# Optimization experiments

Hardware: AMD Instinct MI355X
Metric: run time of the kernel (lower is better)

Reference implementation:

```python
import jax, jax.numpy as jnp
import numpy as np

B, GX, GY = 4, 480, 360
C_IN, C_OUT = 64, 32
N = 480000

def setup_inputs() -> dict:
    key = jax.random.key(0)
    k1, k2, k3, k4, k5 = jax.random.split(key, 5)
    pt_fea = jax.random.normal(k1, (N, C_IN), dtype=jnp.float32)
    pt_ind = jax.random.randint(k2, (N, 2), 0, 360, dtype=jnp.int32)
    batch_idx = jax.random.randint(k3, (N,), 0, B, dtype=jnp.int32)
    W_comp = jax.random.normal(k4, (C_IN, C_OUT), dtype=jnp.float32) * 0.1
    b_comp = jax.random.normal(k5, (C_OUT,), dtype=jnp.float32) * 0.1
    return {"pt_fea": pt_fea, "pt_ind": pt_ind, "batch_idx": batch_idx,
            "W_comp": W_comp, "b_comp": b_comp}

def reference(pt_fea, pt_ind, batch_idx, W_comp, b_comp):
    # Linearized voxel key: (batch, x, y) -> flat segment id.
    # torch.unique + scatter_max over unique voxels followed by fancy-index
    # scatter into a zero grid is equivalent to a dense segment_max with
    # empty voxels forced to zero.
    seg = (batch_idx.astype(jnp.int32) * (GX * GY)
           + pt_ind[:, 0] * GY + pt_ind[:, 1])  # [N]
    num_seg = B * GX * GY
    pooled = jax.ops.segment_max(pt_fea, seg, num_segments=num_seg)  # [BV, C_IN]
    cnt = jax.ops.segment_sum(jnp.ones((pt_fea.shape[0],), jnp.float32), seg,
                              num_segments=num_seg)  # [BV]
    occupied = (cnt > 0)[:, None]
    pooled = jnp.where(occupied, pooled, 0.0)  # neutralize -inf of empty voxels
    # fea_compression: Linear + ReLU, applied to occupied voxels only
    comp = jax.nn.relu(pooled @ W_comp + b_comp)  # [BV, C_OUT]
    comp = jnp.where(occupied, comp, 0.0)
    out = comp.reshape(B, GX, GY, C_OUT)
    return jnp.transpose(out, (0, 3, 1, 2))  # [B, C_OUT, GX, GY]
```

## Files before the change

### kernel.cpp

```cpp
#include <hip/hip_runtime.h>

#define GXGY  172800
#define NSEG  691200
#define NBLK  10800
#define CIN   64
#define COUT  32
#define VPB   64
#define PSTR  65
#define CAP   96
#define SPILLCAP 8192


__device__ __forceinline__ unsigned fkey(float f) {
    unsigned u = __float_as_uint(f);
    return (u & 0x80000000u) ? ~u : (u | 0x80000000u);
}
__device__ __forceinline__ float funkey(unsigned k) {
    unsigned u = (k & 0x80000000u) ? (k ^ 0x80000000u) : ~k;
    return __uint_as_float(u);
}

__global__ __launch_bounds__(256) void bin_kernel(
    const int* __restrict__ ind,
    const int* __restrict__ bidx,
    int*       __restrict__ bCnt,
    int*       __restrict__ spillCnt,
    int*       __restrict__ bucket,
    int2*      __restrict__ spill,
    int N)
{
    int i = blockIdx.x * 256 + threadIdx.x;
    if (i >= N) return;
    int2 xy = ((const int2*)ind)[i];
    int seg = bidx[i] * GXGY + xy.x * 360 + xy.y;
    int blk = seg >> 6;
    int enc = (i << 6) | (seg & 63);
    int pos = atomicAdd(&bCnt[blk], 1);
    if (pos < CAP) {
        bucket[blk * CAP + pos] = enc;
    } else {
        int sp = atomicAdd(spillCnt, 1);
        if (sp < SPILLCAP) spill[sp] = make_int2(blk, enc);
    }
}

__global__ __launch_bounds__(256) void pool_compress_kernel(
    const float* __restrict__ fea,
    const int*   __restrict__ bCnt,
    const int*   __restrict__ spillCnt,
    const int*   __restrict__ bucket,
    const int2*  __restrict__ spill,
    const float* __restrict__ W,
    const float* __restrict__ bias,
    float*       __restrict__ out)
{
    __shared__ __align__(16) unsigned sK[VPB * PSTR];
    __shared__ int sIds[CAP];

    int tid = threadIdx.x;
    int blk = blockIdx.x;
    int vbase = blk * VPB;

    {
        int4 z = make_int4(0, 0, 0, 0);
        #pragma unroll
        for (int j = 0; j < 5; ++j) {
            int idx = tid + j * 256;
            if (idx < (VPB * PSTR) / 4) ((int4*)sK)[idx] = z;
        }
    }

    int nb = min(bCnt[blk], CAP);
    if (tid < nb) sIds[tid] = bucket[blk * CAP + tid];
    __syncthreads();

    int sg = tid >> 4;
    int sl = tid & 15;
    for (int r0 = sg; r0 < nb; r0 += 64) {
        int r1 = min(r0 + 16, nb - 1);
        int r2 = min(r0 + 32, nb - 1);
        int r3 = min(r0 + 48, nb - 1);
        int e0 = sIds[r0], e1 = sIds[r1], e2 = sIds[r2], e3 = sIds[r3];
        int l0 = e0 & 63, l1 = e1 & 63, l2 = e2 & 63, l3 = e3 & 63;
        float4 t0 = ((const float4*)(fea + (size_t)(e0 >> 6) * CIN))[sl];
        float4 t1 = ((const float4*)(fea + (size_t)(e1 >> 6) * CIN))[sl];
        float4 t2 = ((const float4*)(fea + (size_t)(e2 >> 6) * CIN))[sl];
        float4 t3 = ((const float4*)(fea + (size_t)(e3 >> 6) * CIN))[sl];

        unsigned* p0 = &sK[l0 * PSTR + sl * 4];
        atomicMax(p0 + 0, fkey(t0.x)); atomicMax(p0 + 1, fkey(t0.y));
        atomicMax(p0 + 2, fkey(t0.z)); atomicMax(p0 + 3, fkey(t0.w));
        unsigned* p1 = &sK[l1 * PSTR + sl * 4];
        atomicMax(p1 + 0, fkey(t1.x)); atomicMax(p1 + 1, fkey(t1.y));
        atomicMax(p1 + 2, fkey(t1.z)); atomicMax(p1 + 3, fkey(t1.w));
        unsigned* p2 = &sK[l2 * PSTR + sl * 4];
        atomicMax(p2 + 0, fkey(t2.x)); atomicMax(p2 + 1, fkey(t2.y));
        atomicMax(p2 + 2, fkey(t2.z)); atomicMax(p2 + 3, fkey(t2.w));
        unsigned* p3 = &sK[l3 * PSTR + sl * 4];
        atomicMax(p3 + 0, fkey(t3.x)); atomicMax(p3 + 1, fkey(t3.y));
        atomicMax(p3 + 2, fkey(t3.z)); atomicMax(p3 + 3, fkey(t3.w));
    }

    int nsp = spillCnt[0];
    if (nsp > 0) {
        int ns = min(nsp, SPILLCAP);
        for (int j = 0; j < ns; ++j) {
            int2 e = spill[j];
            if (e.x == blk && tid < 16) {
                int lv = e.y & 63;
                float4 t = ((const float4*)(fea + (size_t)(e.y >> 6) * CIN))[tid];
                unsigned* p = &sK[lv * PSTR + tid * 4];
                atomicMax(p + 0, fkey(t.x)); atomicMax(p + 1, fkey(t.y));
                atomicMax(p + 2, fkey(t.z)); atomicMax(p + 3, fkey(t.w));
            }
        }
    }
    __syncthreads();

    int wid  = tid >> 6;
    int lane = tid & 63;
    int lv = lane;
    int g  = __builtin_amdgcn_readfirstlane(wid);
    int b  = vbase / GXGY;
    int rem = vbase - b * GXGY + lv;

    const float* Wg = W + g * 8;
    const float* bg = bias + g * 8;

    const unsigned* row = &sK[lv * PSTR];
    unsigned occk = row[0];

    float res[8];
    if (occk != 0u) {
        float acc[8];
        #pragma unroll
        for (int c = 0; c < 8; ++c) acc[c] = bg[c];
        #pragma unroll
        for (int m = 0; m < 8; ++m) {
            unsigned kk0 = row[m * 8 + 0], kk1 = row[m * 8 + 1];
            unsigned kk2 = row[m * 8 + 2], kk3 = row[m * 8 + 3];
            unsigned kk4 = row[m * 8 + 4], kk5 = row[m * 8 + 5];
            unsigned kk6 = row[m * 8 + 6], kk7 = row[m * 8 + 7];
            float p0 = funkey(kk0), p1 = funkey(kk1);
            float p2 = funkey(kk2), p3 = funkey(kk3);
            float p4 = funkey(kk4), p5 = funkey(kk5);
            float p6 = funkey(kk6), p7 = funkey(kk7);
            const float* Wm = Wg + (m * 8) * COUT;
            #pragma unroll
            for (int c = 0; c < 8; ++c) {
                float a = acc[c];
                a = fmaf(p0, Wm[0 * COUT + c], a);
                a = fmaf(p1, Wm[1 * COUT + c], a);
                a = fmaf(p2, Wm[2 * COUT + c], a);
                a = fmaf(p3, Wm[3 * COUT + c], a);
                a = fmaf(p4, Wm[4 * COUT + c], a);
                a = fmaf(p5, Wm[5 * COUT + c], a);
                a = fmaf(p6, Wm[6 * COUT + c], a);
                a = fmaf(p7, Wm[7 * COUT + c], a);
                acc[c] = a;
            }
        }
        #pragma unroll
        for (int c = 0; c < 8; ++c) res[c] = fmaxf(acc[c], 0.0f);
    } else {
        #pragma unroll
        for (int c = 0; c < 8; ++c) res[c] = 0.0f;
    }

    float* op = out + (size_t)b * COUT * GXGY + (size_t)g * 8 * GXGY + rem;
    #pragma unroll
    for (int c = 0; c < 8; ++c) op[c * GXGY] = res[c];
}

extern "C" void kernel_launch(void* const* d_in, const int* in_sizes, int n_in,
                              void* d_out, int out_size, void* d_ws, size_t ws_size,
                              hipStream_t stream)
{
    const float* fea  = (const float*)d_in[0];
    const int*   ind  = (const int*)d_in[1];
    const int*   bidx = (const int*)d_in[2];
    const float* W    = (const float*)d_in[3];
    const float* bias = (const float*)d_in[4];
    float*       out  = (float*)d_out;

    int N = in_sizes[0] / CIN;

    int* bCnt     = (int*)d_ws;
    int* spillCnt = bCnt + NBLK;
    int* bucket   = bCnt + 10816;
    int2* spill   = (int2*)(bucket + NBLK * CAP);

    hipMemsetAsync(bCnt, 0, 10816 * sizeof(int), stream);
    bin_kernel<<<(N + 255) / 256, 256, 0, stream>>>(ind, bidx, bCnt, spillCnt,
                                                    bucket, spill, N);
    pool_compress_kernel<<<NBLK, 256, 0, stream>>>(fea, bCnt, spillCnt, bucket,
                                                   spill, W, bias, out);
}
```

Before: 279.4 us.

## Make pool kernel persistent with software-pipelined prefetch of next tile's features

Converts the pooling/compression kernel to a persistent grid of 2048 blocks that loop over voxel tiles with a stride. While the current tile is being compressed and written, the bucket ids and the first feature rows of the next tile are loaded into a double-buffered shared id array and registers. The aim is to hide gather latency and cut per-block launch overhead. The cost is extra barriers per tile, more register pressure, and fewer independent blocks to hide latency through occupancy.

```diff
diff --git a/kernel.cpp b/kernel.cpp
--- a/kernel.cpp
+++ b/kernel.cpp
@@ -9,6 +9,7 @@
 #define PSTR  65
 #define CAP   96
 #define SPILLCAP 8192
+#define GRID  2048
 
 
 __device__ __forceinline__ unsigned fkey(float f) {
@@ -55,11 +56,17 @@
     float*       __restrict__ out)
 {
     __shared__ __align__(16) unsigned sK[VPB * PSTR];
-    __shared__ int sIds[CAP];
-
-    int tid = threadIdx.x;
-    int blk = blockIdx.x;
-    int vbase = blk * VPB;
+    __shared__ int sIds[2][CAP];
+
+    int tid  = threadIdx.x;
+    int sg   = tid >> 4;
+    int sl   = tid & 15;
+    int wid  = tid >> 6;
+    int lane = tid & 63;
+    int g    = __builtin_amdgcn_readfirstlane(wid);
+    const float* Wg = W + g * 8;
+    const float* bg = bias + g * 8;
+    int nsp = spillCnt[0];
 
     {
         int4 z = make_int4(0, 0, 0, 0);
@@ -69,107 +76,149 @@
             if (idx < (VPB * PSTR) / 4) ((int4*)sK)[idx] = z;
         }
     }
-
-    int nb = min(bCnt[blk], CAP);
-    if (tid < nb) sIds[tid] = bucket[blk * CAP + tid];
+    int tile   = blockIdx.x;
+    int nb_cur = min(bCnt[tile], CAP);
+    if (tid < nb_cur) sIds[0][tid] = bucket[tile * CAP + tid];
+    int nxt    = tile + GRID;
+    int nb_nxt = (nxt < NBLK) ? min(bCnt[nxt], CAP) : 0;
     __syncthreads();
 
-    int sg = tid >> 4;
-    int sl = tid & 15;
-    for (int r0 = sg; r0 < nb; r0 += 64) {
-        int r1 = min(r0 + 16, nb - 1);
-        int r2 = min(r0 + 32, nb - 1);
-        int r3 = min(r0 + 48, nb - 1);
-        int e0 = sIds[r0], e1 = sIds[r1], e2 = sIds[r2], e3 = sIds[r3];
-        int l0 = e0 & 63, l1 = e1 & 63, l2 = e2 & 63, l3 = e3 & 63;
-        float4 t0 = ((const float4*)(fea + (size_t)(e0 >> 6) * CIN))[sl];
-        float4 t1 = ((const float4*)(fea + (size_t)(e1 >> 6) * CIN))[sl];
-        float4 t2 = ((const float4*)(fea + (size_t)(e2 >> 6) * CIN))[sl];
-        float4 t3 = ((const float4*)(fea + (size_t)(e3 >> 6) * CIN))[sl];
-
-        unsigned* p0 = &sK[l0 * PSTR + sl * 4];
-        atomicMax(p0 + 0, fkey(t0.x)); atomicMax(p0 + 1, fkey(t0.y));
-        atomicMax(p0 + 2, fkey(t0.z)); atomicMax(p0 + 3, fkey(t0.w));
-        unsigned* p1 = &sK[l1 * PSTR + sl * 4];
-        atomicMax(p1 + 0, fkey(t1.x)); atomicMax(p1 + 1, fkey(t1.y));
-        atomicMax(p1 + 2, fkey(t1.z)); atomicMax(p1 + 3, fkey(t1.w));
-        unsigned* p2 = &sK[l2 * PSTR + sl * 4];
-        atomicMax(p2 + 0, fkey(t2.x)); atomicMax(p2 + 1, fkey(t2.y));
-        atomicMax(p2 + 2, fkey(t2.z)); atomicMax(p2 + 3, fkey(t2.w));
-        unsigned* p3 = &sK[l3 * PSTR + sl * 4];
-        atomicMax(p3 + 0, fkey(t3.x)); atomicMax(p3 + 1, fkey(t3.y));
-        atomicMax(p3 + 2, fkey(t3.z)); atomicMax(p3 + 3, fkey(t3.w));
-    }
-
-    int nsp = spillCnt[0];
-    if (nsp > 0) {
-        int ns = min(nsp, SPILLCAP);
-        for (int j = 0; j < ns; ++j) {
-            int2 e = spill[j];
-            if (e.x == blk && tid < 16) {
-                int lv = e.y & 63;
-                float4 t = ((const float4*)(fea + (size_t)(e.y >> 6) * CIN))[tid];
-                unsigned* p = &sK[lv * PSTR + tid * 4];
+    int buf = 0;
+    int e0 = 0, e1 = 0, e2 = 0, e3 = 0;
+    float4 t0, t1, t2, t3;
+    if (nb_cur > 0) {
+        int nbm = nb_cur - 1;
+        e0 = sIds[0][min(sg,      nbm)];
+        e1 = sIds[0][min(sg + 16, nbm)];
+        e2 = sIds[0][min(sg + 32, nbm)];
+        e3 = sIds[0][min(sg + 48, nbm)];
+        t0 = ((const float4*)(fea + (size_t)(e0 >> 6) * CIN))[sl];
+        t1 = ((const float4*)(fea + (size_t)(e1 >> 6) * CIN))[sl];
+        t2 = ((const float4*)(fea + (size_t)(e2 >> 6) * CIN))[sl];
+        t3 = ((const float4*)(fea + (size_t)(e3 >> 6) * CIN))[sl];
+    }
+
+    while (tile < NBLK) {
+        if (nb_cur > 0) {
+            int l0 = e0 & 63, l1 = e1 & 63, l2 = e2 & 63, l3 = e3 & 63;
+            unsigned* p0 = &sK[l0 * PSTR + sl * 4];
+            atomicMax(p0 + 0, fkey(t0.x)); atomicMax(p0 + 1, fkey(t0.y));
+            atomicMax(p0 + 2, fkey(t0.z)); atomicMax(p0 + 3, fkey(t0.w));
+            unsigned* p1 = &sK[l1 * PSTR + sl * 4];
+            atomicMax(p1 + 0, fkey(t1.x)); atomicMax(p1 + 1, fkey(t1.y));
+            atomicMax(p1 + 2, fkey(t1.z)); atomicMax(p1 + 3, fkey(t1.w));
+            unsigned* p2 = &sK[l2 * PSTR + sl * 4];
+            atomicMax(p2 + 0, fkey(t2.x)); atomicMax(p2 + 1, fkey(t2.y));
+            atomicMax(p2 + 2, fkey(t2.z)); atomicMax(p2 + 3, fkey(t2.w));
+            unsigned* p3 = &sK[l3 * PSTR + sl * 4];
+            atomicMax(p3 + 0, fkey(t3.x)); atomicMax(p3 + 1, fkey(t3.y));
+            atomicMax(p3 + 2, fkey(t3.z)); atomicMax(p3 + 3, fkey(t3.w));
+            for (int r = sg + 64; r < nb_cur; r += 16) {
+                int e = sIds[buf][r];
+                int l = e & 63;
+                float4 t = ((const float4*)(fea + (size_t)(e >> 6) * CIN))[sl];
+                unsigned* p = &sK[l * PSTR + sl * 4];
                 atomicMax(p + 0, fkey(t.x)); atomicMax(p + 1, fkey(t.y));
                 atomicMax(p + 2, fkey(t.z)); atomicMax(p + 3, fkey(t.w));
             }
         }
-    }
-    __syncthreads();
-
-    int wid  = tid >> 6;
-    int lane = tid & 63;
-    int lv = lane;
-    int g  = __builtin_amdgcn_readfirstlane(wid);
-    int b  = vbase / GXGY;
-    int rem = vbase - b * GXGY + lv;
-
-    const float* Wg = W + g * 8;
-    const float* bg = bias + g * 8;
-
-    const unsigned* row = &sK[lv * PSTR];
-    unsigned occk = row[0];
-
-    float res[8];
-    if (occk != 0u) {
-        float acc[8];
-        #pragma unroll
-        for (int c = 0; c < 8; ++c) acc[c] = bg[c];
-        #pragma unroll
-        for (int m = 0; m < 8; ++m) {
-            unsigned kk0 = row[m * 8 + 0], kk1 = row[m * 8 + 1];
-            unsigned kk2 = row[m * 8 + 2], kk3 = row[m * 8 + 3];
-            unsigned kk4 = row[m * 8 + 4], kk5 = row[m * 8 + 5];
-            unsigned kk6 = row[m * 8 + 6], kk7 = row[m * 8 + 7];
-            float p0 = funkey(kk0), p1 = funkey(kk1);
-            float p2 = funkey(kk2), p3 = funkey(kk3);
-            float p4 = funkey(kk4), p5 = funkey(kk5);
-            float p6 = funkey(kk6), p7 = funkey(kk7);
-            const float* Wm = Wg + (m * 8) * COUT;
+        if (nsp > 0) {
+            int ns = min(nsp, SPILLCAP);
+            for (int j = 0; j < ns; ++j) {
+                int2 e = spill[j];
+                if (e.x == tile && tid < 16) {
+                    int lv = e.y & 63;
+                    float4 t = ((const float4*)(fea + (size_t)(e.y >> 6) * CIN))[tid];
+                    unsigned* p = &sK[lv * PSTR + tid * 4];
+                    atomicMax(p + 0, fkey(t.x)); atomicMax(p + 1, fkey(t.y));
+                    atomicMax(p + 2, fkey(t.z)); atomicMax(p + 3, fkey(t.w));
+                }
+            }
+        }
+        if (tid < nb_nxt) sIds[buf ^ 1][tid] = bucket[nxt * CAP + tid];
+        int nxt2    = nxt + GRID;
+        int nb_nxt2 = (nxt2 < NBLK) ? min(bCnt[nxt2], CAP) : 0;
+        __syncthreads();
+
+        int ne0 = 0, ne1 = 0, ne2 = 0, ne3 = 0;
+        float4 nt0, nt1, nt2, nt3;
+        if (nb_nxt > 0) {
+            int nbm = nb_nxt - 1;
+            int bn  = buf ^ 1;
+            ne0 = sIds[bn][min(sg,      nbm)];
+            ne1 = sIds[bn][min(sg + 16, nbm)];
+            ne2 = sIds[bn][min(sg + 32, nbm)];
+            ne3 = sIds[bn][min(sg + 48, nbm)];
+            nt0 = ((const float4*)(fea + (size_t)(ne0 >> 6) * CIN))[sl];
+            nt1 = ((const float4*)(fea + (size_t)(ne1 >> 6) * CIN))[sl];
+            nt2 = ((const float4*)(fea + (size_t)(ne2 >> 6) * CIN))[sl];
+            nt3 = ((const float4*)(fea + (size_t)(ne3 >> 6) * CIN))[sl];
+        }
+
+        {
+            int vbase = tile * VPB;
+            int b   = vbase / GXGY;
+            int rem = vbase - b * GXGY + lane;
+            const unsigned* row = &sK[lane * PSTR];
+            unsigned occk = row[0];
+            float res[8];
+            if (occk != 0u) {
+                float acc[8];
+                #pragma unroll
+                for (int c = 0; c < 8; ++c) acc[c] = bg[c];
+                #pragma unroll
+                for (int m = 0; m < 8; ++m) {
+                    unsigned kk0 = row[m * 8 + 0], kk1 = row[m * 8 + 1];
+                    unsigned kk2 = row[m * 8 + 2], kk3 = row[m * 8 + 3];
+                    unsigned kk4 = row[m * 8 + 4], kk5 = row[m * 8 + 5];
+                    unsigned kk6 = row[m * 8 + 6], kk7 = row[m * 8 + 7];
+                    float p0 = funkey(kk0), p1 = funkey(kk1);
+                    float p2 = funkey(kk2), p3 = funkey(kk3);
+                    float p4 = funkey(kk4), p5 = funkey(kk5);
+                    float p6 = funkey(kk6), p7 = funkey(kk7);
+                    const float* Wm = Wg + (m * 8) * COUT;
+                    #pragma unroll
+                    for (int c = 0; c < 8; ++c) {
+                        float a = acc[c];
+                        a = fmaf(p0, Wm[0 * COUT + c], a);
+                        a = fmaf(p1, Wm[1 * COUT + c], a);
+                        a = fmaf(p2, Wm[2 * COUT + c], a);
+                        a = fmaf(p3, Wm[3 * COUT + c], a);
+                        a = fmaf(p4, Wm[4 * COUT + c], a);
+                        a = fmaf(p5, Wm[5 * COUT + c], a);
+                        a = fmaf(p6, Wm[6 * COUT + c], a);
+                        a = fmaf(p7, Wm[7 * COUT + c], a);
+                        acc[c] = a;
+                    }
+                }
+                #pragma unroll
+                for (int c = 0; c < 8; ++c) res[c] = fmaxf(acc[c], 0.0f);
+            } else {
+                #pragma unroll
+                for (int c = 0; c < 8; ++c) res[c] = 0.0f;
+            }
+            float* op = out + (size_t)b * COUT * GXGY + (size_t)g * 8 * GXGY + rem;
             #pragma unroll
-            for (int c = 0; c < 8; ++c) {
-                float a = acc[c];
-                a = fmaf(p0, Wm[0 * COUT + c], a);
-                a = fmaf(p1, Wm[1 * COUT + c], a);
-                a = fmaf(p2, Wm[2 * COUT + c], a);
-                a = fmaf(p3, Wm[3 * COUT + c], a);
-                a = fmaf(p4, Wm[4 * COUT + c], a);
-                a = fmaf(p5, Wm[5 * COUT + c], a);
-                a = fmaf(p6, Wm[6 * COUT + c], a);
-                a = fmaf(p7, Wm[7 * COUT + c], a);
-                acc[c] = a;
-            }
-        }
-        #pragma unroll
-        for (int c = 0; c < 8; ++c) res[c] = fmaxf(acc[c], 0.0f);
-    } else {
-        #pragma unroll
-        for (int c = 0; c < 8; ++c) res[c] = 0.0f;
-    }
-
-    float* op = out + (size_t)b * COUT * GXGY + (size_t)g * 8 * GXGY + rem;
-    #pragma unroll
-    for (int c = 0; c < 8; ++c) op[c * GXGY] = res[c];
+            for (int c = 0; c < 8; ++c) op[c * GXGY] = res[c];
+        }
+        __syncthreads();
+
+        {
+            int4 z = make_int4(0, 0, 0, 0);
+            #pragma unroll
+            for (int j = 0; j < 5; ++j) {
+                int idx = tid + j * 256;
+                if (idx < (VPB * PSTR) / 4) ((int4*)sK)[idx] = z;
+            }
+        }
+        __syncthreads();
+
+        tile = nxt; nxt = nxt2;
+        nb_cur = nb_nxt; nb_nxt = nb_nxt2;
+        e0 = ne0; e1 = ne1; e2 = ne2; e3 = ne3;
+        t0 = nt0; t1 = nt1; t2 = nt2; t3 = nt3;
+        buf ^= 1;
+    }
 }
 
 extern "C" void kernel_launch(void* const* d_in, const int* in_sizes, int n_in,
@@ -193,6 +242,6 @@
     hipMemsetAsync(bCnt, 0, 10816 * sizeof(int), stream);
     bin_kernel<<<(N + 255) / 256, 256, 0, stream>>>(ind, bidx, bCnt, spillCnt,
                                                     bucket, spill, N);
-    pool_compress_kernel<<<NBLK, 256, 0, stream>>>(fea, bCnt, spillCnt, bucket,
+    pool_compress_kernel<<<GRID, 256, 0, stream>>>(fea, bCnt, spillCnt, bucket,
                                                    spill, W, bias, out);
 }
```

Result: no change. 278.4 us (-0.4%).
